# Performance work log

Measured on AMD Instinct MI355X. Metric: run time of the kernel, lower is better.

## Reference

```python
import jax, jax.numpy as jnp
import numpy as np

B, S, D, L, INNER = 16, 512, 768, 20, 64
NEG = 1e12


def setup_inputs() -> dict:
    key = jax.random.key(0)
    k1, k2, k3 = jax.random.split(key, 3)
    x = jax.random.normal(k1, (B, S, D), jnp.float32)
    attention_mask = jnp.ones((B, S), jnp.int32)
    w1 = jax.random.normal(k2, (D, 2 * INNER), jnp.float32) * 0.02
    b1 = jnp.zeros((2 * INNER,), jnp.float32)
    w2 = jax.random.normal(k3, (D, 2 * L), jnp.float32) * 0.02
    b2 = jnp.zeros((2 * L,), jnp.float32)
    return {"x": x, "attention_mask": attention_mask, "w1": w1, "b1": b1, "w2": w2, "b2": b2}


def _rope(v, cos_pos, sin_pos):
    # interleaved rotation: [-v1, v0, -v3, v2, ...]
    v2 = jnp.stack([-v[..., 1::2], v[..., ::2]], axis=-1).reshape(v.shape)
    return v * cos_pos + v2 * sin_pos


def reference(x, attention_mask, w1, b1, w2, b2):
    Bc, Sc, _ = x.shape
    out1 = x @ w1 + b1                       # [B,S,2*INNER]
    qw, kw = out1[..., ::2], out1[..., 1::2]  # each [B,S,INNER]
    # sinusoidal position embedding, interleaved sin/cos -> [1,S,INNER]
    pos_ids = jnp.arange(Sc, dtype=jnp.float32)[:, None]
    idx = jnp.arange(INNER // 2, dtype=jnp.float32)
    freqs = jnp.power(10000.0, -2.0 * idx / INNER)
    ang = pos_ids * freqs                    # [S, INNER//2]
    pos = jnp.stack([jnp.sin(ang), jnp.cos(ang)], axis=-1).reshape(1, Sc, INNER)
    cos_pos = jnp.repeat(pos[..., 1::2], 2, axis=-1)
    sin_pos = jnp.repeat(pos[..., ::2], 2, axis=-1)
    qw = _rope(qw, cos_pos, sin_pos)
    kw = _rope(kw, cos_pos, sin_pos)
    logits = jnp.einsum('bmd,bnd->bmn', qw, kw) / jnp.sqrt(jnp.float32(INNER))  # [B,S,S]
    dense = jnp.swapaxes(x @ w2 + b2, 1, 2) / 2.0  # [B,2L,S]
    # broadcast per-label start/end biases -> [B,L,S,S]
    logits = logits[:, None] + dense[:, ::2, None, :] + dense[:, 1::2, :, None]
    m = attention_mask.astype(logits.dtype)
    m1 = m[:, None, :, None]
    m2 = m[:, None, None, :]
    logits = logits * m1 - NEG * (1.0 - m1)
    logits = logits * m2 - NEG * (1.0 - m2)
    tril = jnp.tril(jnp.ones((Sc, Sc), logits.dtype), -1)
    logits = logits - tril * NEG
    probs = jax.nn.sigmoid(logits)
    return logits, probs
```

## Files before the change

### kernel.cpp

```cpp
#include <hip/hip_runtime.h>

typedef float v4 __attribute__((ext_vector_type(4)));
typedef float v2 __attribute__((ext_vector_type(2)));
typedef int  iv4 __attribute__((ext_vector_type(4)));

#define NEGV 1000000000000.0f
#define SEQ 512
#define NL 20
#define LOGITS_ELEMS (16 * 20 * 512 * 512)

__global__ __launch_bounds__(256)
void prep_kernel(const float* __restrict__ x, const float* __restrict__ w1,
                 const float* __restrict__ b1, const float* __restrict__ w2,
                 const float* __restrict__ b2,
                 float* __restrict__ qw, float* __restrict__ kw,
                 float* __restrict__ dense)
{
    __shared__ float xs[32][36];
    __shared__ float wsm[32][64];

    const int tid = threadIdx.x;
    const int jb = blockIdx.x;
    const int m0 = blockIdx.y * 32;
    const int j0 = jb * 64;

    const int tx = tid & 15;
    const int ty = tid >> 4;

    const int sxm = tid >> 3;
    const int sxk = (tid & 7) * 4;
    const int swk = tid >> 3;
    const int swn = (tid & 7) * 8;

    float acc0[4] = {0.f, 0.f, 0.f, 0.f};
    float acc1[4] = {0.f, 0.f, 0.f, 0.f};

    for (int k0 = 0; k0 < 768; k0 += 32) {
        v4 xa = *(const v4*)&x[(size_t)(m0 + sxm) * 768 + k0 + sxk];
        v4 wa, wb;
        if (jb < 2) {
            wa = *(const v4*)&w1[(size_t)(k0 + swk) * 128 + j0 + swn];
            wb = *(const v4*)&w1[(size_t)(k0 + swk) * 128 + j0 + swn + 4];
        } else if (swn < 40) {
            wa = *(const v4*)&w2[(size_t)(k0 + swk) * 40 + swn];
            wb = *(const v4*)&w2[(size_t)(k0 + swk) * 40 + swn + 4];
        } else {
            wa = 0.0f; wb = 0.0f;
        }
        __syncthreads();
        *(v4*)&xs[sxm][sxk] = xa;
        *(v4*)&wsm[swk][swn] = wa;
        *(v4*)&wsm[swk][swn + 4] = wb;
        __syncthreads();
#pragma unroll
        for (int k = 0; k < 32; k += 4) {
            v4 a0 = *(const v4*)&xs[ty][k];
            v4 a1 = *(const v4*)&xs[ty + 16][k];
            v4 bv0 = *(const v4*)&wsm[k + 0][tx * 4];
            v4 bv1 = *(const v4*)&wsm[k + 1][tx * 4];
            v4 bv2 = *(const v4*)&wsm[k + 2][tx * 4];
            v4 bv3 = *(const v4*)&wsm[k + 3][tx * 4];
#pragma unroll
            for (int j = 0; j < 4; ++j) {
                acc0[j] += a0[0] * bv0[j] + a0[1] * bv1[j] + a0[2] * bv2[j] + a0[3] * bv3[j];
                acc1[j] += a1[0] * bv0[j] + a1[1] * bv1[j] + a1[2] * bv2[j] + a1[3] * bv3[j];
            }
        }
    }

    if (jb < 2) {
        const int p = (j0 >> 2) + tx;
        const float fr = __powf(10000.0f, (float)(-2 * p) / 64.0f);
        v4 bb = *(const v4*)&b1[j0 + tx * 4];
#pragma unroll
        for (int i = 0; i < 2; ++i) {
            const float* acc = (i == 0) ? acc0 : acc1;
            const int mrow = m0 + ty + 16 * i;
            const int s = mrow & 511;
            float ang = (float)s * fr;
            float sn = sinf(ang), cs = cosf(ang);
            float q0 = acc[0] + bb[0];
            float k0v = acc[1] + bb[1];
            float q1 = acc[2] + bb[2];
            float k1v = acc[3] + bb[3];
            v2 qo, ko;
            qo[0] = q0 * cs - q1 * sn;  qo[1] = q1 * cs + q0 * sn;
            ko[0] = k0v * cs - k1v * sn; ko[1] = k1v * cs + k0v * sn;
            *(v2*)&qw[(size_t)mrow * 64 + 2 * p] = qo;
            *(v2*)&kw[(size_t)mrow * 64 + 2 * p] = ko;
        }
    } else if (tx < 10) {
        v4 bb = *(const v4*)&b2[tx * 4];
#pragma unroll
        for (int i = 0; i < 2; ++i) {
            const float* acc = (i == 0) ? acc0 : acc1;
            const int mrow = m0 + ty + 16 * i;
            const int bi = mrow >> 9;
            const int s = mrow & 511;
#pragma unroll
            for (int j = 0; j < 4; ++j) {
                dense[(size_t)(bi * 40 + tx * 4 + j) * 512 + s] = (acc[j] + bb[j]) * 0.5f;
            }
        }
    }
}

__global__ __launch_bounds__(256)
void fused_kernel(const float* __restrict__ qw, const float* __restrict__ kw,
                  const float* __restrict__ dense, const int* __restrict__ mask,
                  float* __restrict__ outL, float* __restrict__ outP)
{
    __shared__ float qkS[32][260];
    __shared__ float qwL[32][68];
    __shared__ float kwT[64][64];
    __shared__ float dOs[20][32];
    __shared__ float mMs[32];

    const int tid = threadIdx.x;
    const int nT0 = blockIdx.x * 256;
    const int m0  = blockIdx.y * 32;
    const int b   = blockIdx.z;

    {
        const int m = tid >> 3, kk = (tid & 7) * 8;
        v4 a = *(const v4*)&qw[(size_t)(b * SEQ + m0 + m) * 64 + kk];
        v4 c = *(const v4*)&qw[(size_t)(b * SEQ + m0 + m) * 64 + kk + 4];
        *(v4*)&qwL[m][kk] = a;
        *(v4*)&qwL[m][kk + 4] = c;
    }
#pragma unroll
    for (int t = 0; t < 3; ++t) {
        int flat = t * 256 + tid;
        if (flat < 640) {
            int l = flat >> 5, m = flat & 31;
            dOs[l][m] = dense[(size_t)(b * 40 + 2 * l + 1) * 512 + m0 + m];
        }
    }
    if (tid < 32) mMs[tid] = (float)mask[b * SEQ + m0 + tid];

    const int txc = tid & 15;
    const int r   = tid >> 4;
    const int kn  = tid >> 2;
    const int kkk = (tid & 3) * 16;

    for (int nc = 0; nc < 4; ++nc) {
        const int n0 = nT0 + nc * 64;
        v4 kv[4];
#pragma unroll
        for (int t = 0; t < 4; ++t)
            kv[t] = *(const v4*)&kw[(size_t)(b * SEQ + n0 + kn) * 64 + kkk + 4 * t];
        __syncthreads();
#pragma unroll
        for (int t = 0; t < 4; ++t) {
            kwT[kkk + 4 * t + 0][kn] = kv[t][0];
            kwT[kkk + 4 * t + 1][kn] = kv[t][1];
            kwT[kkk + 4 * t + 2][kn] = kv[t][2];
            kwT[kkk + 4 * t + 3][kn] = kv[t][3];
        }
        __syncthreads();

        float acc0[4] = {0.f, 0.f, 0.f, 0.f};
        float acc1[4] = {0.f, 0.f, 0.f, 0.f};
#pragma unroll
        for (int k = 0; k < 64; k += 4) {
            v4 a0 = *(const v4*)&qwL[r][k];
            v4 a1 = *(const v4*)&qwL[r + 16][k];
            v4 bv0 = *(const v4*)&kwT[k + 0][txc * 4];
            v4 bv1 = *(const v4*)&kwT[k + 1][txc * 4];
            v4 bv2 = *(const v4*)&kwT[k + 2][txc * 4];
            v4 bv3 = *(const v4*)&kwT[k + 3][txc * 4];
#pragma unroll
            for (int j = 0; j < 4; ++j) {
                acc0[j] += a0[0] * bv0[j] + a0[1] * bv1[j] + a0[2] * bv2[j] + a0[3] * bv3[j];
                acc1[j] += a1[0] * bv0[j] + a1[1] * bv1[j] + a1[2] * bv2[j] + a1[3] * bv3[j];
            }
        }
        v4 o0, o1;
#pragma unroll
        for (int j = 0; j < 4; ++j) { o0[j] = acc0[j] * 0.125f; o1[j] = acc1[j] * 0.125f; }
        *(v4*)&qkS[r][nc * 64 + txc * 4] = o0;
        *(v4*)&qkS[r + 16][nc * 64 + txc * 4] = o1;
    }
    __syncthreads();

    const int c    = tid & 63;
    const int half = tid >> 6;
    const int gn0  = nT0 + c * 4;

    iv4 mi = *(const iv4*)&mask[b * SEQ + gn0];
    v4 mNv, cN;
#pragma unroll
    for (int j = 0; j < 4; ++j) {
        mNv[j] = (float)mi[j];
        cN[j] = -NEGV * (1.0f - mNv[j]);
    }

    const float* dePtr = &dense[(size_t)(b * 40) * 512 + gn0];
    v4 de = *(const v4*)dePtr;
    for (int l = 0; l < NL; ++l) {
        const v4 deC = de;
        if (l + 1 < NL)
            de = *(const v4*)(dePtr + (size_t)(2 * (l + 1)) * 512);
        const size_t lbase = ((size_t)(b * NL + l) * SEQ + m0) * SEQ + gn0;
#pragma unroll
        for (int it = 0; it < 8; ++it) {
            const int row  = it * 4 + half;
            const int grow = m0 + row;
            v4 qk = *(const v4*)&qkS[row][c * 4];
            const float doo = dOs[l][row];
            const float mM  = mMs[row];
            const float cM  = -NEGV * (1.0f - mM);
            v4 lv, pv;
#pragma unroll
            for (int j = 0; j < 4; ++j) {
                float v = qk[j] + deC[j] + doo;
                v = v * mM + cM;
                v = v * mNv[j] + cN[j];
                if (grow > gn0 + j) v -= NEGV;
                lv[j] = v;
                pv[j] = __builtin_amdgcn_rcpf(1.0f + __expf(-v));
            }
            const size_t base = lbase + (size_t)row * SEQ;
            *(v4*)&outL[base] = lv;
            *(v4*)&outP[base] = pv;
        }
    }
}

extern "C" void kernel_launch(void* const* d_in, const int* in_sizes, int n_in,
                              void* d_out, int out_size, void* d_ws, size_t ws_size,
                              hipStream_t stream) {
    (void)in_sizes; (void)n_in; (void)out_size; (void)ws_size;
    const float* x    = (const float*)d_in[0];
    const int*   mask = (const int*)d_in[1];
    const float* w1   = (const float*)d_in[2];
    const float* b1   = (const float*)d_in[3];
    const float* w2   = (const float*)d_in[4];
    const float* b2   = (const float*)d_in[5];

    float* ws = (float*)d_ws;
    float* qw    = ws;
    float* kw    = ws + 524288;
    float* dense = ws + 1048576;

    float* outL = (float*)d_out;
    float* outP = outL + (size_t)LOGITS_ELEMS;

    prep_kernel<<<dim3(3, 256), 256, 0, stream>>>(x, w1, b1, w2, b2, qw, kw, dense);
    fused_kernel<<<dim3(2, 16, 16), 256, 0, stream>>>(qw, kw, dense, mask, outL, outP);
}
```

Baseline: 736.4 us.

## Keep QK tile in registers and shrink column tile to 128

Drops the shared-memory staging of the transposed K tile and the QK score tile. Each thread now computes a 4x4 block of scores straight from global K rows and shared Q rows, keeping the results in registers for the 20-label output loop. The column tile per block is halved to 128, so the grid doubles to 1024 blocks for better occupancy and less LDS traffic. The cost is uncoalesced, strided global reads of K and recomputing the QK product in twice as many blocks, but the kernel is dominated by the output writes.

After: 737.6 us. About the same (+0.2%).

```diff
diff --git a/kernel.cpp b/kernel.cpp
--- a/kernel.cpp
+++ b/kernel.cpp
@@ -110,14 +110,12 @@
                   const float* __restrict__ dense, const int* __restrict__ mask,
                   float* __restrict__ outL, float* __restrict__ outP)
 {
-    __shared__ float qkS[32][260];
     __shared__ float qwL[32][68];
-    __shared__ float kwT[64][64];
     __shared__ float dOs[20][32];
     __shared__ float mMs[32];
 
     const int tid = threadIdx.x;
-    const int nT0 = blockIdx.x * 256;
+    const int nT0 = blockIdx.x * 128;
     const int m0  = blockIdx.y * 32;
     const int b   = blockIdx.z;
 
@@ -137,55 +135,40 @@
         }
     }
     if (tid < 32) mMs[tid] = (float)mask[b * SEQ + m0 + tid];
-
-    const int txc = tid & 15;
-    const int r   = tid >> 4;
-    const int kn  = tid >> 2;
-    const int kkk = (tid & 3) * 16;
-
-    for (int nc = 0; nc < 4; ++nc) {
-        const int n0 = nT0 + nc * 64;
-        v4 kv[4];
-#pragma unroll
-        for (int t = 0; t < 4; ++t)
-            kv[t] = *(const v4*)&kw[(size_t)(b * SEQ + n0 + kn) * 64 + kkk + 4 * t];
-        __syncthreads();
-#pragma unroll
-        for (int t = 0; t < 4; ++t) {
-            kwT[kkk + 4 * t + 0][kn] = kv[t][0];
-            kwT[kkk + 4 * t + 1][kn] = kv[t][1];
-            kwT[kkk + 4 * t + 2][kn] = kv[t][2];
-            kwT[kkk + 4 * t + 3][kn] = kv[t][3];
-        }
-        __syncthreads();
-
-        float acc0[4] = {0.f, 0.f, 0.f, 0.f};
-        float acc1[4] = {0.f, 0.f, 0.f, 0.f};
-#pragma unroll
-        for (int k = 0; k < 64; k += 4) {
-            v4 a0 = *(const v4*)&qwL[r][k];
-            v4 a1 = *(const v4*)&qwL[r + 16][k];
-            v4 bv0 = *(const v4*)&kwT[k + 0][txc * 4];
-            v4 bv1 = *(const v4*)&kwT[k + 1][txc * 4];
-            v4 bv2 = *(const v4*)&kwT[k + 2][txc * 4];
-            v4 bv3 = *(const v4*)&kwT[k + 3][txc * 4];
-#pragma unroll
-            for (int j = 0; j < 4; ++j) {
-                acc0[j] += a0[0] * bv0[j] + a0[1] * bv1[j] + a0[2] * bv2[j] + a0[3] * bv3[j];
-                acc1[j] += a1[0] * bv0[j] + a1[1] * bv1[j] + a1[2] * bv2[j] + a1[3] * bv3[j];
-            }
-        }
-        v4 o0, o1;
-#pragma unroll
-        for (int j = 0; j < 4; ++j) { o0[j] = acc0[j] * 0.125f; o1[j] = acc1[j] * 0.125f; }
-        *(v4*)&qkS[r][nc * 64 + txc * 4] = o0;
-        *(v4*)&qkS[r + 16][nc * 64 + txc * 4] = o1;
-    }
     __syncthreads();
 
-    const int c    = tid & 63;
-    const int half = tid >> 6;
+    const int c    = tid & 31;
+    const int half = tid >> 5;
     const int gn0  = nT0 + c * 4;
+
+    float acc[4][4] = {};
+    const float* kwB = &kw[(size_t)(b * SEQ + gn0) * 64];
+#pragma unroll
+    for (int k = 0; k < 64; k += 4) {
+        v4 bv0 = *(const v4*)&kwB[0 * 64 + k];
+        v4 bv1 = *(const v4*)&kwB[1 * 64 + k];
+        v4 bv2 = *(const v4*)&kwB[2 * 64 + k];
+        v4 bv3 = *(const v4*)&kwB[3 * 64 + k];
+        v4 a0 = *(const v4*)&qwL[0 * 8 + half][k];
+        v4 a1 = *(const v4*)&qwL[1 * 8 + half][k];
+        v4 a2 = *(const v4*)&qwL[2 * 8 + half][k];
+        v4 a3 = *(const v4*)&qwL[3 * 8 + half][k];
+#pragma unroll
+        for (int kk = 0; kk < 4; ++kk) {
+            acc[0][0] += a0[kk] * bv0[kk]; acc[0][1] += a0[kk] * bv1[kk];
+            acc[0][2] += a0[kk] * bv2[kk]; acc[0][3] += a0[kk] * bv3[kk];
+            acc[1][0] += a1[kk] * bv0[kk]; acc[1][1] += a1[kk] * bv1[kk];
+            acc[1][2] += a1[kk] * bv2[kk]; acc[1][3] += a1[kk] * bv3[kk];
+            acc[2][0] += a2[kk] * bv0[kk]; acc[2][1] += a2[kk] * bv1[kk];
+            acc[2][2] += a2[kk] * bv2[kk]; acc[2][3] += a2[kk] * bv3[kk];
+            acc[3][0] += a3[kk] * bv0[kk]; acc[3][1] += a3[kk] * bv1[kk];
+            acc[3][2] += a3[kk] * bv2[kk]; acc[3][3] += a3[kk] * bv3[kk];
+        }
+    }
+#pragma unroll
+    for (int i = 0; i < 4; ++i)
+#pragma unroll
+        for (int j = 0; j < 4; ++j) acc[i][j] *= 0.125f;
 
     iv4 mi = *(const iv4*)&mask[b * SEQ + gn0];
     v4 mNv, cN;
@@ -203,17 +186,16 @@
             de = *(const v4*)(dePtr + (size_t)(2 * (l + 1)) * 512);
         const size_t lbase = ((size_t)(b * NL + l) * SEQ + m0) * SEQ + gn0;
 #pragma unroll
-        for (int it = 0; it < 8; ++it) {
-            const int row  = it * 4 + half;
+        for (int i = 0; i < 4; ++i) {
+            const int row  = i * 8 + half;
             const int grow = m0 + row;
-            v4 qk = *(const v4*)&qkS[row][c * 4];
             const float doo = dOs[l][row];
             const float mM  = mMs[row];
             const float cM  = -NEGV * (1.0f - mM);
             v4 lv, pv;
 #pragma unroll
             for (int j = 0; j < 4; ++j) {
-                float v = qk[j] + deC[j] + doo;
+                float v = acc[i][j] + deC[j] + doo;
                 v = v * mM + cM;
                 v = v * mNv[j] + cN[j];
                 if (grow > gn0 + j) v -= NEGV;
@@ -247,5 +229,5 @@
     float* outP = outL + (size_t)LOGITS_ELEMS;
 
     prep_kernel<<<dim3(3, 256), 256, 0, stream>>>(x, w1, b1, w2, b2, qw, kw, dense);
-    fused_kernel<<<dim3(2, 16, 16), 256, 0, stream>>>(qw, kw, dense, mask, outL, outP);
+    fused_kernel<<<dim3(4, 16, 16), 256, 0, stream>>>(qw, kw, dense, mask, outL, outP);
 }
```
